# Performance work log

Hardware: AMD Instinct MI355X
Metric: run time of the kernel (lower is better)

## Reference

```python
import jax, jax.numpy as jnp
import numpy as np

B, SQ, SKV, D, H = 2, 2048, 2048, 1024, 16
HD = D // H  # 64
ROPE_BASE = 10000.0


def setup_inputs() -> dict:
    key = jax.random.key(0)
    ks = jax.random.split(key, 6)
    s = 1.0 / np.sqrt(D)  # keep activations well-scaled
    return {
        "x_q": jax.random.normal(ks[0], (B, SQ, D), jnp.float32),
        "x_kv": jax.random.normal(ks[1], (B, SKV, D), jnp.float32),
        "wq": jax.random.normal(ks[2], (D, D), jnp.float32) * s,
        "bq": jnp.zeros((D,), jnp.float32),
        "wk": jax.random.normal(ks[3], (D, D), jnp.float32) * s,
        "bk": jnp.zeros((D,), jnp.float32),
        "wv": jax.random.normal(ks[4], (D, D), jnp.float32) * s,
        "bv": jnp.zeros((D,), jnp.float32),
        "wo": jax.random.normal(ks[5], (D, D), jnp.float32) * s,
        "bo": jnp.zeros((D,), jnp.float32),
    }


def _rope_interleaved(x):
    # x: [B, S, H, HD]; sequential positions starting at 0 (GPT-NeoX style)
    s, hd = x.shape[1], x.shape[-1]
    dim = hd // 2
    freqs = jnp.exp(-jnp.arange(dim, dtype=x.dtype) * jnp.log(jnp.asarray(ROPE_BASE, x.dtype)) / dim)
    ang = jnp.arange(s, dtype=x.dtype)[:, None] * freqs[None, :]  # [S, dim]
    cos = jnp.cos(ang)[None, :, None, :]
    sin = jnp.sin(ang)[None, :, None, :]
    xe, xo = x[..., ::2], x[..., 1::2]
    re = xe * cos - xo * sin
    ro = xe * sin + xo * cos
    return jnp.stack([re, ro], axis=-1).reshape(x.shape)


def reference(x_q, x_kv, wq, bq, wk, bk, wv, bv, wo, bo):
    b, sq, _ = x_q.shape
    skv = x_kv.shape[1]
    q = (jnp.einsum("bsd,ed->bse", x_q, wq) + bq).reshape(b, sq, H, HD)
    k = (jnp.einsum("bsd,ed->bse", x_kv, wk) + bk).reshape(b, skv, H, HD)
    v = (jnp.einsum("bsd,ed->bse", x_kv, wv) + bv).reshape(b, skv, H, HD)
    q = _rope_interleaved(q)
    k = _rope_interleaved(k)
    scores = jnp.einsum("bqhd,bkhd->bhqk", q, k) / jnp.sqrt(jnp.asarray(HD, q.dtype))
    attn = jax.nn.softmax(scores, axis=-1)
    ctx = jnp.einsum("bhqk,bkhd->bqhd", attn, v).reshape(b, sq, D)
    return jnp.einsum("bsd,ed->bse", ctx, wo) + bo
```

## Files before the change

### kernel.cpp

```cpp
#include <hip/hip_runtime.h>
#include <cstdint>

typedef __attribute__((ext_vector_type(8))) short bf16x8;
typedef __attribute__((ext_vector_type(4))) float f32x4;
typedef __attribute__((ext_vector_type(4))) unsigned int u32x4;

#define DEV static __device__ __forceinline__

DEV unsigned short f2bf(float f) {
  unsigned int u = __builtin_bit_cast(unsigned int, f);
  u += 0x7FFFu + ((u >> 16) & 1u);
  return (unsigned short)(u >> 16);
}
#if __has_builtin(__builtin_amdgcn_cvt_pk_bf16_f32)
DEV unsigned int pkbf(float a, float b) {
  auto v = __builtin_amdgcn_cvt_pk_bf16_f32(a, b);
  return __builtin_bit_cast(unsigned int, v);
}
#else
DEV unsigned int pkbf(float a, float b) {
  return (unsigned int)f2bf(a) | ((unsigned int)f2bf(b) << 16);
}
#endif
#if __has_builtin(__builtin_amdgcn_exp2f)
#define EXP2(x) __builtin_amdgcn_exp2f(x)
#else
#define EXP2(x) exp2f(x)
#endif
DEV float bfl(unsigned int u) { return __builtin_bit_cast(float, u << 16); }
DEV float bfh(unsigned int u) { return __builtin_bit_cast(float, u & 0xFFFF0000u); }

DEV void async_copy16(const unsigned short* g, unsigned short* l) {
  __builtin_amdgcn_global_load_lds(
      (const __attribute__((address_space(1))) unsigned int*)(uintptr_t)g,
      (__attribute__((address_space(3))) unsigned int*)(uintptr_t)l,
      16, 0, 0);
}

#if __has_builtin(__builtin_amdgcn_permlane32_swap) && \
    __has_builtin(__builtin_amdgcn_permlane16_swap)
DEV void pswap(unsigned a, unsigned b, unsigned& w0, unsigned& w2, int lane) {
  (void)lane;
  auto pq = __builtin_amdgcn_permlane32_swap((int)a, (int)b, false, false);
  auto wz = __builtin_amdgcn_permlane16_swap(pq[0], pq[1], false, false);
  w0 = (unsigned)wz[0];
  w2 = (unsigned)wz[1];
}
#else
DEV void pswap(unsigned a, unsigned b, unsigned& w0, unsigned& w2, int lane) {
  int q = lane >> 4, l = lane & 15;
  int src0 = ((q & 1) << 5) + l;
  int a0 = __shfl((int)a, src0), b0 = __shfl((int)b, src0);
  int a2 = __shfl((int)a, src0 + 16), b2 = __shfl((int)b, src0 + 16);
  w0 = (unsigned)(q < 2 ? a0 : b0);
  w2 = (unsigned)(q < 2 ? a2 : b2);
}
#endif

__global__ __launch_bounds__(256) void cvt8(
    const float* __restrict__ w0, const float* __restrict__ w1,
    const float* __restrict__ w2, const float* __restrict__ w3,
    const float* __restrict__ x0, const float* __restrict__ x1,
    unsigned short* __restrict__ wsb, unsigned short* __restrict__ xb)
{
  int id = blockIdx.x * 256 + threadIdx.x;
  const float* src;
  unsigned short* dp;
  int off;
  if (id < (1 << 20)) {
    int m = id >> 18;
    off = (id & 0x3FFFF) << 2;
    src = m == 0 ? w0 : m == 1 ? w1 : m == 2 ? w2 : w3;
    dp = wsb + (((size_t)m) << 20) + off;
  } else {
    int id2 = id - (1 << 20);
    int m = id2 >> 20;
    off = (id2 & 0xFFFFF) << 2;
    src = m ? x1 : x0;
    dp = xb + (((size_t)m) << 22) + off;
  }
  float4 v = *(const float4*)(src + off);
  uint2 o;
  o.x = pkbf(v.x, v.y);
  o.y = pkbf(v.z, v.w);
  *(uint2*)dp = o;
}

__global__ __launch_bounds__(256) void gemm_qkv_bf(
    const unsigned short* __restrict__ xqb,
    const unsigned short* __restrict__ xkvb,
    const unsigned short* __restrict__ wbase,
    const float* __restrict__ bq, const float* __restrict__ bk,
    const float* __restrict__ bv,
    unsigned short* __restrict__ outq, unsigned short* __restrict__ outk,
    unsigned short* __restrict__ outvT)
{
  constexpr int K = 1024;
  __shared__ unsigned short As[2][64 * 64];
  __shared__ unsigned short Bs[2][128 * 64];
  const int id = blockIdx.x;
  const int sw_id = (id & 7) * 192 + (id >> 3);
  const int z = sw_id >> 9;
  const int r = sw_id & 511;
  const int mBase = (r >> 3) << 6, nBase = (r & 7) << 7;

  const unsigned short* X = (z == 0) ? xqb : xkvb;
  const unsigned short* Wb = wbase + (((size_t)z) << 20);
  const float* bias = (z == 0) ? bq : (z == 1) ? bk : bv;

  const int tid = threadIdx.x;
  const int wave = tid >> 6, lane = tid & 63;
  const int quad = lane >> 4, l16 = lane & 15;
  const int wm = (wave >> 1) << 5, wn = (wave & 1) << 6;

  const int La0 = tid, La1 = 256 + tid;
  const int ra0 = La0 >> 3, ca0 = ((La0 & 7) ^ (ra0 & 7)) << 3;
  const int ra1 = La1 >> 3, ca1 = ((La1 & 7) ^ (ra1 & 7)) << 3;
  const int Lb0 = tid,        rb0 = Lb0 >> 3, cb0 = ((Lb0 & 7) ^ (rb0 & 7)) << 3;
  const int Lb1 = 256 + tid,  rb1 = Lb1 >> 3, cb1 = ((Lb1 & 7) ^ (rb1 & 7)) << 3;
  const int Lb2 = 512 + tid,  rb2 = Lb2 >> 3, cb2 = ((Lb2 & 7) ^ (rb2 & 7)) << 3;
  const int Lb3 = 768 + tid,  rb3 = Lb3 >> 3, cb3 = ((Lb3 & 7) ^ (rb3 & 7)) << 3;

  f32x4 acc[2][4] = {};

#define QKV_STAGE(kt, bi)                                                      \
  do {                                                                         \
    const int k0_ = (kt) * 64;                                                 \
    async_copy16(X + (size_t)(mBase + ra0) * K + k0_ + ca0, &As[bi][La0 * 8]); \
    async_copy16(X + (size_t)(mBase + ra1) * K + k0_ + ca1, &As[bi][La1 * 8]); \
    async_copy16(Wb + (size_t)(nBase + rb0) * K + k0_ + cb0, &Bs[bi][Lb0 * 8]);\
    async_copy16(Wb + (size_t)(nBase + rb1) * K + k0_ + cb1, &Bs[bi][Lb1 * 8]);\
    async_copy16(Wb + (size_t)(nBase + rb2) * K + k0_ + cb2, &Bs[bi][Lb2 * 8]);\
    async_copy16(Wb + (size_t)(nBase + rb3) * K + k0_ + cb3, &Bs[bi][Lb3 * 8]);\
  } while (0)

  QKV_STAGE(0, 0);
  __syncthreads();

  const int swz = l16 & 7;
  for (int it = 0; it < 16; ++it) {
    const int cur = it & 1;
    if (it < 15)
      QKV_STAGE(it + 1, cur ^ 1);
#pragma unroll
    for (int kd = 0; kd < 2; ++kd) {
      const int cs = (((kd * 4 + quad) ^ swz) << 3);
      bf16x8 af[2], bff[4];
#pragma unroll
      for (int t = 0; t < 2; ++t)
        af[t] = *(const bf16x8*)&As[cur][(wm + t * 16 + l16) * 64 + cs];
#pragma unroll
      for (int t = 0; t < 4; ++t)
        bff[t] = *(const bf16x8*)&Bs[cur][(wn + t * 16 + l16) * 64 + cs];
#pragma unroll
      for (int mt = 0; mt < 2; ++mt)
#pragma unroll
        for (int nt = 0; nt < 4; ++nt)
          acc[mt][nt] = __builtin_amdgcn_mfma_f32_16x16x32_bf16(af[mt], bff[nt], acc[mt][nt], 0, 0, 0);
    }
    __syncthreads();
  }
#undef QKV_STAGE

  if (z < 2) {
    unsigned short* out = z ? outk : outq;
    const float qs = z ? 1.0f : 0.18033688011112042f;
    const int sBlk = (mBase & 2047) + wm + quad * 4;
#pragma unroll
    for (int nt = 0; nt < 4; ++nt) {
      int n = nBase + wn + nt * 16 + l16;
      float bv2 = bias[n];
      int h = n >> 6, hd = n & 63;
      int i = hd >> 1;
      int parity = n & 1;
      float f = exp2f(-(float)i * 0.4152410118609203f);
      float sf, cf;
      sincosf(f, &sf, &cf);
#pragma unroll
      for (int mt = 0; mt < 2; ++mt) {
        float ang = (float)(sBlk + mt * 16) * f;
        float s, c;
        sincosf(ang, &s, &c);
#pragma unroll
        for (int j = 0; j < 4; ++j) {
          float v = acc[mt][nt][j] + bv2;
          float pv = __shfl_xor(v, 1);
          float ce = c * qs;
          float se = (parity ? s : -s) * qs;
          float outv = v * ce + pv * se;
          int m = mBase + wm + mt * 16 + quad * 4 + j;
          int b = m >> 11, sv = m & 2047;
          out[(((size_t)(b * 16 + h) * 2048 + sv) << 6) + hd] = f2bf(outv);
          float c2 = c * cf - s * sf;
          s = s * cf + c * sf;
          c = c2;
        }
      }
    }
  } else {
#pragma unroll
    for (int nt = 0; nt < 4; ++nt) {
      int n = nBase + wn + nt * 16 + l16;
      float bv2 = bias[n];
      int h = n >> 6, hd = n & 63;
#pragma unroll
      for (int mt = 0; mt < 2; ++mt) {
        int m0 = mBase + wm + mt * 16 + quad * 4;
        int b = m0 >> 11, s = m0 & 2047;
        uint2 o;
        o.x = pkbf(acc[mt][nt][0] + bv2, acc[mt][nt][1] + bv2);
        o.y = pkbf(acc[mt][nt][2] + bv2, acc[mt][nt][3] + bv2);
        *(uint2*)&outvT[(((size_t)(b * 16 + h) * 64 + hd) << 11) + s] = o;
      }
    }
  }
}

__global__ __launch_bounds__(512) void attn_v9(
    const unsigned short* __restrict__ Qg,
    const unsigned short* __restrict__ Kg,
    const unsigned short* __restrict__ VT,
    unsigned short* __restrict__ Opart,
    float* __restrict__ lbuf)
{
  __shared__ unsigned short Ks[2][64 * 64];
  __shared__ unsigned short Vs[3][64 * 64];
  const int tid = threadIdx.x, wave = tid >> 6, lane = tid & 63;
  const int quad = lane >> 4, l16 = lane & 15;
  const int bh = blockIdx.x & 31;
  const int qt = (blockIdx.x >> 5) & 7;
  const int kvs = blockIdx.x >> 8;
  const int q0 = qt * 256 + wave * 32;
  const unsigned short* Qb = Qg + ((size_t)bh << 17);
  const unsigned short* Kb = Kg + ((size_t)bh << 17);
  const unsigned short* Vb = VT + ((size_t)bh << 17);

  const int L0 = tid;
  const int r0 = L0 >> 3;
  const int c0 = ((L0 & 7) ^ (r0 & 7)) << 3;

  bf16x8 qf[2][2];
#pragma unroll
  for (int mq = 0; mq < 2; ++mq)
#pragma unroll
    for (int kd = 0; kd < 2; ++kd)
      qf[mq][kd] = *(const bf16x8*)(Qb + (size_t)(q0 + mq * 16 + l16) * 64 + kd * 32 + quad * 8);

  bf16x8 onesf;
#pragma unroll
  for (int i = 0; i < 8; ++i) onesf[i] = (short)0x3F80;

  f32x4 oacc[4][2] = {};
  f32x4 laccv[2] = {};
  bf16x8 pfp[2][2];

  const int kvbeg = kvs << 10;
  const int swz = l16 & 7;

  async_copy16(Kb + (size_t)(kvbeg + r0) * 64 + c0, &Ks[0][L0 * 8]);
  async_copy16(Vb + (size_t)r0 * 2048 + kvbeg + c0, &Vs[0][L0 * 8]);
  __syncthreads();

  for (int t = 0; t < 16; ++t) {
    const int kcur = t & 1;
    if (t < 15) {
      const int kv0 = kvbeg + (t + 1) * 64;
      async_copy16(Kb + (size_t)(kv0 + r0) * 64 + c0, &Ks[kcur ^ 1][L0 * 8]);
      async_copy16(Vb + (size_t)r0 * 2048 + kv0 + c0, &Vs[(t + 1) % 3][L0 * 8]);
    }

    if (t > 0) {
      const unsigned short* Vp = Vs[(t - 1) % 3];
      __builtin_amdgcn_s_setprio(1);
#pragma unroll
      for (int ks = 0; ks < 2; ++ks) {
#pragma unroll
        for (int th = 0; th < 4; ++th) {
          bf16x8 vf = *(const bf16x8*)&Vp[(th * 16 + l16) * 64 + (((ks * 4 + quad) ^ swz) << 3)];
#pragma unroll
          for (int mq = 0; mq < 2; ++mq)
            oacc[th][mq] = __builtin_amdgcn_mfma_f32_16x16x32_bf16(vf, pfp[ks][mq], oacc[th][mq], 0, 0, 0);
        }
#pragma unroll
        for (int mq = 0; mq < 2; ++mq)
          laccv[mq] = __builtin_amdgcn_mfma_f32_16x16x32_bf16(onesf, pfp[ks][mq], laccv[mq], 0, 0, 0);
      }
      __builtin_amdgcn_s_setprio(0);
    }

    const unsigned short* Kc = Ks[kcur];
    f32x4 st[4][2] = {};
    __builtin_amdgcn_s_setprio(1);
#pragma unroll
    for (int kd = 0; kd < 2; ++kd)
#pragma unroll
      for (int tk = 0; tk < 4; ++tk) {
        bf16x8 kf = *(const bf16x8*)&Kc[(tk * 16 + l16) * 64 + (((kd * 4 + quad) ^ swz) << 3)];
#pragma unroll
        for (int mq = 0; mq < 2; ++mq)
          st[tk][mq] = __builtin_amdgcn_mfma_f32_16x16x32_bf16(kf, qf[mq][kd], st[tk][mq], 0, 0, 0);
      }
    __builtin_amdgcn_s_setprio(0);

#pragma unroll
    for (int mq = 0; mq < 2; ++mq)
#pragma unroll
      for (int tk = 0; tk < 4; ++tk)
#pragma unroll
        for (int jr = 0; jr < 4; ++jr)
          st[tk][mq][jr] = EXP2(st[tk][mq][jr]);

#pragma unroll
    for (int ks = 0; ks < 2; ++ks)
#pragma unroll
      for (int mq = 0; mq < 2; ++mq) {
        u32x4 pw;
#pragma unroll
        for (int w = 0; w < 2; ++w) {
          unsigned a = pkbf(st[2 * ks][mq][2 * w], st[2 * ks][mq][2 * w + 1]);
          unsigned b = pkbf(st[2 * ks + 1][mq][2 * w], st[2 * ks + 1][mq][2 * w + 1]);
          unsigned w0, w2;
          pswap(a, b, w0, w2, lane);
          pw[w] = w0;
          pw[w + 2] = w2;
        }
        pfp[ks][mq] = __builtin_bit_cast(bf16x8, pw);
      }

    __syncthreads();
  }

  {
    const unsigned short* Vp = Vs[15 % 3];
    __builtin_amdgcn_s_setprio(1);
#pragma unroll
    for (int ks = 0; ks < 2; ++ks) {
#pragma unroll
      for (int th = 0; th < 4; ++th) {
        bf16x8 vf = *(const bf16x8*)&Vp[(th * 16 + l16) * 64 + (((ks * 4 + quad) ^ swz) << 3)];
#pragma unroll
        for (int mq = 0; mq < 2; ++mq)
          oacc[th][mq] = __builtin_amdgcn_mfma_f32_16x16x32_bf16(vf, pfp[ks][mq], oacc[th][mq], 0, 0, 0);
      }
#pragma unroll
      for (int mq = 0; mq < 2; ++mq)
        laccv[mq] = __builtin_amdgcn_mfma_f32_16x16x32_bf16(onesf, pfp[ks][mq], laccv[mq], 0, 0, 0);
    }
    __builtin_amdgcn_s_setprio(0);
  }

  const int b = bh >> 4, h = bh & 15;
  unsigned short* Od = Opart + (((size_t)kvs) << 22);
#pragma unroll
  for (int mq = 0; mq < 2; ++mq) {
    int s = q0 + mq * 16 + l16;
    if (quad == 0)
      lbuf[(kvs * 32 + bh) * 2048 + s] = laccv[mq][0];
#pragma unroll
    for (int th = 0; th < 4; ++th) {
      uint2 o;
      o.x = pkbf(oacc[th][mq][0], oacc[th][mq][1]);
      o.y = pkbf(oacc[th][mq][2], oacc[th][mq][3]);
      *(uint2*)&Od[((size_t)(b * 2048 + s) << 10) + h * 64 + th * 16 + quad * 4] = o;
    }
  }
}

__global__ __launch_bounds__(256) void combine_kernel(
    const unsigned short* __restrict__ Opart, const float* __restrict__ lbuf,
    unsigned short* __restrict__ ctx)
{
  int idx = blockIdx.x * 256 + threadIdx.x;
  int m = idx >> 9;
  int c2 = idx & 511;
  int b = m >> 11, s = m & 2047;
  int h = c2 >> 5;
  int bh = b * 16 + h;
  float la = lbuf[bh * 2048 + s];
  float lb = lbuf[(32 + bh) * 2048 + s];
  float r = 1.0f / (la + lb);
  unsigned int ua = ((const unsigned int*)Opart)[idx];
  unsigned int ub = ((const unsigned int*)Opart)[(1u << 21) + idx];
  float o0 = (bfl(ua) + bfl(ub)) * r;
  float o1 = (bfh(ua) + bfh(ub)) * r;
  ((unsigned int*)ctx)[idx] = pkbf(o0, o1);
}

__global__ __launch_bounds__(256) void gemm_o_bf(
    const unsigned short* __restrict__ X,
    const unsigned short* __restrict__ Wb,
    const float* __restrict__ bias,
    float* __restrict__ out)
{
  constexpr int K = 1024;
  __shared__ unsigned short As[3][64 * 32];
  __shared__ unsigned short Bs[3][128 * 32];
  const int id = blockIdx.x;
  const int sw_id = (id & 7) * 64 + (id >> 3);
  const int mBase = (sw_id >> 3) << 6, nBase = (sw_id & 7) << 7;

  const int tid = threadIdx.x;
  const int wave = tid >> 6, lane = tid & 63;
  const int quad = lane >> 4, l16 = lane & 15;
  const int wm = (wave >> 1) << 5, wn = (wave & 1) << 6;

  const int La = tid, ra = La >> 2, ca = ((La & 3) ^ (ra & 3)) << 3;
  const int Lb1 = 256 + tid, rb1 = Lb1 >> 2, cb1 = ((Lb1 & 3) ^ (rb1 & 3)) << 3;

  f32x4 acc[2][4] = {};

#define O_STAGE(kt, bi)                                                        \
  do {                                                                         \
    const int k0_ = (kt) * 32;                                                 \
    async_copy16(X + (size_t)(mBase + ra) * K + k0_ + ca, &As[bi][La * 8]);    \
    async_copy16(Wb + (size_t)(nBase + ra) * K + k0_ + ca, &Bs[bi][La * 8]);   \
    async_copy16(Wb + (size_t)(nBase + rb1) * K + k0_ + cb1, &Bs[bi][Lb1 * 8]);\
  } while (0)

  O_STAGE(0, 0);
  O_STAGE(1, 1);

  const int sw = (quad ^ (l16 & 3)) << 3;
  for (int it = 0; it < 32; ++it) {
    if (it < 31)
      asm volatile("s_waitcnt vmcnt(3)" ::: "memory");
    else
      asm volatile("s_waitcnt vmcnt(0)" ::: "memory");
    __builtin_amdgcn_s_barrier();
    if (it < 30)
      O_STAGE(it + 2, (it + 2) % 3);
    const int cur = it % 3;
    bf16x8 af[2], bff[4];
#pragma unroll
    for (int t = 0; t < 2; ++t)
      af[t] = *(const bf16x8*)&As[cur][(wm + t * 16 + l16) * 32 + sw];
#pragma unroll
    for (int t = 0; t < 4; ++t)
      bff[t] = *(const bf16x8*)&Bs[cur][(wn + t * 16 + l16) * 32 + sw];
#pragma unroll
    for (int mt = 0; mt < 2; ++mt)
#pragma unroll
      for (int nt = 0; nt < 4; ++nt)
        acc[mt][nt] = __builtin_amdgcn_mfma_f32_16x16x32_bf16(af[mt], bff[nt], acc[mt][nt], 0, 0, 0);
  }
#undef O_STAGE

#pragma unroll
  for (int nt = 0; nt < 4; ++nt) {
    int n = nBase + wn + nt * 16 + l16;
    float bv = bias[n];
#pragma unroll
    for (int mt = 0; mt < 2; ++mt) {
#pragma unroll
      for (int j = 0; j < 4; ++j) {
        int m = mBase + wm + mt * 16 + quad * 4 + j;
        out[((size_t)m << 10) + n] = acc[mt][nt][j] + bv;
      }
    }
  }
}

extern "C" void kernel_launch(void* const* d_in, const int* in_sizes, int n_in,
                              void* d_out, int out_size, void* d_ws, size_t ws_size,
                              hipStream_t stream) {
  const float* x_q  = (const float*)d_in[0];
  const float* x_kv = (const float*)d_in[1];
  const float* wq   = (const float*)d_in[2];
  const float* bq   = (const float*)d_in[3];
  const float* wk   = (const float*)d_in[4];
  const float* bk   = (const float*)d_in[5];
  const float* wv   = (const float*)d_in[6];
  const float* bv   = (const float*)d_in[7];
  const float* wo   = (const float*)d_in[8];
  const float* bo   = (const float*)d_in[9];

  unsigned short* base = (unsigned short*)d_ws;
  unsigned short* ob   = (unsigned short*)d_out;

  unsigned short* wob  = base + (3u << 20);
  unsigned short* k    = base + (4u << 20);
  unsigned short* vT   = base + (8u << 20);
  unsigned short* q    = base + (12u << 20);
  unsigned short* ctx  = q;
  float*          lbuf = (float*)d_ws;
  unsigned short* xqb  = ob;
  unsigned short* xkvb = ob + (4u << 20);
  unsigned short* Opart = ob;
  float* out = (float*)d_out;

  cvt8<<<12288, 256, 0, stream>>>(wq, wk, wv, wo, x_q, x_kv, base, ob);
  gemm_qkv_bf<<<1536, 256, 0, stream>>>(xqb, xkvb, base, bq, bk, bv, q, k, vT);
  attn_v9<<<512, 512, 0, stream>>>(q, k, vT, Opart, lbuf);
  combine_kernel<<<8192, 256, 0, stream>>>(Opart, lbuf, ctx);
  gemm_o_bf<<<512, 256, 0, stream>>>(ctx, wob, bo, out);
}
```

Before: 217.1 us.

## Use double-buffered 64-wide K tiles in output projection GEMM

```diff
diff --git a/kernel.cpp b/kernel.cpp
--- a/kernel.cpp
+++ b/kernel.cpp
@@ -393,8 +393,8 @@
     float* __restrict__ out)
 {
   constexpr int K = 1024;
-  __shared__ unsigned short As[3][64 * 32];
-  __shared__ unsigned short Bs[3][128 * 32];
+  __shared__ unsigned short As[2][64 * 64];
+  __shared__ unsigned short Bs[2][128 * 64];
   const int id = blockIdx.x;
   const int sw_id = (id & 7) * 64 + (id >> 3);
   const int mBase = (sw_id >> 3) << 6, nBase = (sw_id & 7) << 7;
@@ -404,44 +404,52 @@
   const int quad = lane >> 4, l16 = lane & 15;
   const int wm = (wave >> 1) << 5, wn = (wave & 1) << 6;
 
-  const int La = tid, ra = La >> 2, ca = ((La & 3) ^ (ra & 3)) << 3;
-  const int Lb1 = 256 + tid, rb1 = Lb1 >> 2, cb1 = ((Lb1 & 3) ^ (rb1 & 3)) << 3;
+  const int La0 = tid, La1 = 256 + tid;
+  const int ra0 = La0 >> 3, ca0 = ((La0 & 7) ^ (ra0 & 7)) << 3;
+  const int ra1 = La1 >> 3, ca1 = ((La1 & 7) ^ (ra1 & 7)) << 3;
+  const int Lb0 = tid,        rb0 = Lb0 >> 3, cb0 = ((Lb0 & 7) ^ (rb0 & 7)) << 3;
+  const int Lb1 = 256 + tid,  rb1 = Lb1 >> 3, cb1 = ((Lb1 & 7) ^ (rb1 & 7)) << 3;
+  const int Lb2 = 512 + tid,  rb2 = Lb2 >> 3, cb2 = ((Lb2 & 7) ^ (rb2 & 7)) << 3;
+  const int Lb3 = 768 + tid,  rb3 = Lb3 >> 3, cb3 = ((Lb3 & 7) ^ (rb3 & 7)) << 3;
 
   f32x4 acc[2][4] = {};
 
 #define O_STAGE(kt, bi)                                                        \
   do {                                                                         \
-    const int k0_ = (kt) * 32;                                                 \
-    async_copy16(X + (size_t)(mBase + ra) * K + k0_ + ca, &As[bi][La * 8]);    \
-    async_copy16(Wb + (size_t)(nBase + ra) * K + k0_ + ca, &Bs[bi][La * 8]);   \
+    const int k0_ = (kt) * 64;                                                 \
+    async_copy16(X + (size_t)(mBase + ra0) * K + k0_ + ca0, &As[bi][La0 * 8]); \
+    async_copy16(X + (size_t)(mBase + ra1) * K + k0_ + ca1, &As[bi][La1 * 8]); \
+    async_copy16(Wb + (size_t)(nBase + rb0) * K + k0_ + cb0, &Bs[bi][Lb0 * 8]);\
     async_copy16(Wb + (size_t)(nBase + rb1) * K + k0_ + cb1, &Bs[bi][Lb1 * 8]);\
+    async_copy16(Wb + (size_t)(nBase + rb2) * K + k0_ + cb2, &Bs[bi][Lb2 * 8]);\
+    async_copy16(Wb + (size_t)(nBase + rb3) * K + k0_ + cb3, &Bs[bi][Lb3 * 8]);\
   } while (0)
 
   O_STAGE(0, 0);
-  O_STAGE(1, 1);
-
-  const int sw = (quad ^ (l16 & 3)) << 3;
-  for (int it = 0; it < 32; ++it) {
-    if (it < 31)
-      asm volatile("s_waitcnt vmcnt(3)" ::: "memory");
-    else
-      asm volatile("s_waitcnt vmcnt(0)" ::: "memory");
-    __builtin_amdgcn_s_barrier();
-    if (it < 30)
-      O_STAGE(it + 2, (it + 2) % 3);
-    const int cur = it % 3;
-    bf16x8 af[2], bff[4];
-#pragma unroll
-    for (int t = 0; t < 2; ++t)
-      af[t] = *(const bf16x8*)&As[cur][(wm + t * 16 + l16) * 32 + sw];
-#pragma unroll
-    for (int t = 0; t < 4; ++t)
-      bff[t] = *(const bf16x8*)&Bs[cur][(wn + t * 16 + l16) * 32 + sw];
-#pragma unroll
-    for (int mt = 0; mt < 2; ++mt)
-#pragma unroll
-      for (int nt = 0; nt < 4; ++nt)
-        acc[mt][nt] = __builtin_amdgcn_mfma_f32_16x16x32_bf16(af[mt], bff[nt], acc[mt][nt], 0, 0, 0);
+  __syncthreads();
+
+  const int swz = l16 & 7;
+  for (int it = 0; it < 16; ++it) {
+    const int cur = it & 1;
+    if (it < 15)
+      O_STAGE(it + 1, cur ^ 1);
+#pragma unroll
+    for (int kd = 0; kd < 2; ++kd) {
+      const int cs = (((kd * 4 + quad) ^ swz) << 3);
+      bf16x8 af[2], bff[4];
+#pragma unroll
+      for (int t = 0; t < 2; ++t)
+        af[t] = *(const bf16x8*)&As[cur][(wm + t * 16 + l16) * 64 + cs];
+#pragma unroll
+      for (int t = 0; t < 4; ++t)
+        bff[t] = *(const bf16x8*)&Bs[cur][(wn + t * 16 + l16) * 64 + cs];
+#pragma unroll
+      for (int mt = 0; mt < 2; ++mt)
+#pragma unroll
+        for (int nt = 0; nt < 4; ++nt)
+          acc[mt][nt] = __builtin_amdgcn_mfma_f32_16x16x32_bf16(af[mt], bff[nt], acc[mt][nt], 0, 0, 0);
+    }
+    __syncthreads();
   }
 #undef O_STAGE
 
```

Measured after the change: 209.0 us, median of 2. -3.8%, faster.
